# Optimization experiments

Measured on AMD Instinct MI355X. Metric: run time of the kernel, lower is better.

The kernel has to match this reference:

```python
import jax, jax.numpy as jnp
import numpy as np


def setup_inputs() -> dict:
    key = jax.random.key(0)
    k_xyz, k_w1, k_b1, k_w2, k_b2 = jax.random.split(key, 5)
    B, N = 2, 1024
    D_MODEL, N_HEADS = 128, 8
    HID = D_MODEL // 2
    # Kaiming-ish init scale for the tiny MLP weights
    return {
        "xyz": jax.random.normal(k_xyz, (B, 3, N), dtype=jnp.float32),
        "W1": jax.random.normal(k_w1, (3, HID), dtype=jnp.float32) * (1.0 / np.sqrt(3.0)),
        "b1": jax.random.normal(k_b1, (HID,), dtype=jnp.float32) * 0.01,
        "W2": jax.random.normal(k_w2, (HID, N_HEADS), dtype=jnp.float32) * (1.0 / np.sqrt(HID)),
        "b2": jax.random.normal(k_b2, (N_HEADS,), dtype=jnp.float32) * 0.01,
    }


def reference(xyz, W1, b1, W2, b2):
    # xyz: [B, 3, N] -> [B, N, 3]
    pts = jnp.transpose(xyz, (0, 2, 1))
    # pairwise relative positions: rel[b, i, j, :] = pts[b, j] - pts[b, i]
    # (matches xyz.unsqueeze(1) - xyz.unsqueeze(2) in torch)
    rel = pts[:, None, :, :] - pts[:, :, None, :]          # [B, N, N, 3]
    h = jax.nn.relu(jnp.einsum("bijc,ch->bijh", rel, W1) + b1)  # [B, N, N, HID]
    bias = jnp.einsum("bijh,hk->bijk", h, W2) + b2         # [B, N, N, H]
    # permute(0, 3, 1, 2) -> [B, H, N, N]
    return jnp.transpose(bias, (0, 3, 1, 2))
```

## Files before the change

kernel.cpp:

```cpp
#include <hip/hip_runtime.h>
#include <hip/hip_bf16.h>

#define HID   64
#define NHD   8
#define IT    16
#define WAVES 8
#define JTW   32
#define JT    (WAVES*JTW)

typedef _Float16 f16x8 __attribute__((ext_vector_type(8)));
typedef float    f32x4 __attribute__((ext_vector_type(4)));

__global__ __launch_bounds__(WAVES * 64, 4) void relposenc_f16(
    const float* __restrict__ xyz, const float* __restrict__ W1,
    const float* __restrict__ b1,  const float* __restrict__ W2,
    const float* __restrict__ b2,  float* __restrict__ out, int N) {

  __shared__ float    sW1b1[4][HID];
  __shared__ _Float16 sU[IT][HID];

  const int tid  = threadIdx.x;
  const int wave = tid >> 6;
  const int lane = tid & 63;
  const int col  = lane & 15;
  const int hgrp = lane >> 4;
  const int b    = blockIdx.z;
  const int i0   = blockIdx.y * IT;
  const int j0   = blockIdx.x * JT + wave * JTW;

  const float* xb = xyz + (size_t)b * 3 * N;

  if (tid < 4 * HID) {
    int r = tid >> 6, h = tid & 63;
    sW1b1[r][h] = (r < 3) ? W1[r * HID + h] : b1[h];
  }
  for (int t = tid; t < IT * HID; t += WAVES * 64) {
    int ii = t >> 6, h = t & 63;
    int i  = i0 + ii;
    float u = fmaf(xb[i], W1[h],
              fmaf(xb[N + i], W1[HID + h],
                   xb[2 * N + i] * W1[2 * HID + h]));
    sU[ii][h] = (_Float16)u;
  }

  f16x8 aLo[2], aHi[2];
  #pragma unroll
  for (int kb = 0; kb < 2; ++kb)
    #pragma unroll
    for (int e = 0; e < 8; ++e) {
      int h = kb * 32 + hgrp * 8 + e;
      aLo[kb][e] = (_Float16)((col < NHD)  ? W2[h * NHD + col]       : 0.f);
      aHi[kb][e] = (_Float16)((col >= NHD) ? W2[h * NHD + (col - 8)] : 0.f);
    }
  float b2v[4];
  #pragma unroll
  for (int r = 0; r < 4; ++r) b2v[r] = b2[((hgrp & 1) << 2) + r];

  __syncthreads();

  f16x8 aj[2][2];
  #pragma unroll
  for (int t = 0; t < 2; ++t) {
    int j = j0 + t * 16 + col;
    float x0 = xb[j], x1 = xb[N + j], x2 = xb[2 * N + j];
    #pragma unroll
    for (int kb = 0; kb < 2; ++kb)
      #pragma unroll
      for (int e = 0; e < 8; ++e) {
        int h = kb * 32 + hgrp * 8 + e;
        float v = fmaf(x0, sW1b1[0][h],
                  fmaf(x1, sW1b1[1][h],
                  fmaf(x2, sW1b1[2][h], sW1b1[3][h])));
        aj[t][kb][e] = (_Float16)v;
      }
  }

  const size_t jj = (size_t)j0 + col + ((size_t)(lane >> 5) << 4);
  const int kbase = (hgrp & 1) << 2;
  float* outp = out + ((size_t)(b * NHD + kbase) * N + i0) * N + jj;
  const size_t plane = (size_t)N * N;

  const f16x8 z = {0, 0, 0, 0, 0, 0, 0, 0};

  f16x8 nu0 = *(const f16x8*)&sU[0][hgrp * 8];
  f16x8 nu1 = *(const f16x8*)&sU[0][32 + hgrp * 8];

  for (int ii = 0; ii < IT; ++ii) {
    f16x8 u0 = nu0, u1 = nu1;
    if (ii + 1 < IT) {
      nu0 = *(const f16x8*)&sU[ii + 1][hgrp * 8];
      nu1 = *(const f16x8*)&sU[ii + 1][32 + hgrp * 8];
    }

    f16x8 d00 = __builtin_elementwise_max(aj[0][0] - u0, z);
    f16x8 d01 = __builtin_elementwise_max(aj[0][1] - u1, z);
    f16x8 d10 = __builtin_elementwise_max(aj[1][0] - u0, z);
    f16x8 d11 = __builtin_elementwise_max(aj[1][1] - u1, z);

    f32x4 cA = {0.f, 0.f, 0.f, 0.f}, cB = {0.f, 0.f, 0.f, 0.f};
    cA = __builtin_amdgcn_mfma_f32_16x16x32_f16(aLo[0], d00, cA, 0, 0, 0);
    cA = __builtin_amdgcn_mfma_f32_16x16x32_f16(aLo[1], d01, cA, 0, 0, 0);
    cB = __builtin_amdgcn_mfma_f32_16x16x32_f16(aHi[0], d10, cB, 0, 0, 0);
    cB = __builtin_amdgcn_mfma_f32_16x16x32_f16(aHi[1], d11, cB, 0, 0, 0);

    float* p = outp + (size_t)ii * N;
    #pragma unroll
    for (int r = 0; r < 4; ++r) {
      p[(size_t)r * plane] = cA[r] + cB[r] + b2v[r];
    }
  }
}

extern "C" void kernel_launch(void* const* d_in, const int* in_sizes, int n_in,
                              void* d_out, int out_size, void* d_ws, size_t ws_size,
                              hipStream_t stream) {
  const float* xyz = (const float*)d_in[0];
  const float* W1  = (const float*)d_in[1];
  const float* b1  = (const float*)d_in[2];
  const float* W2  = (const float*)d_in[3];
  const float* b2  = (const float*)d_in[4];
  float* out = (float*)d_out;

  const long long in0 = in_sizes[0];
  const int N = (int)((3LL * (long long)out_size) / (8LL * in0));
  const int B = (int)(in0 / (3LL * N));

  dim3 grid(N / JT, N / IT, B);
  relposenc_f16<<<grid, WAVES * 64, 0, stream>>>(xyz, W1, b1, W2, b2, out, N);
}
```

Before: 24.28 us.

## Stage output rows in LDS and write full rows with coalesced 16-byte stores

Each block now covers 2 query rows across all N columns. Results go into a 64KB LDS buffer laid out head-major, and each wave then streams one head's rows to global memory as contiguous float4 stores. Before, lanes issued scattered 4-byte stores. The j-side first layer is now computed with packed f16 FMAs (W1 and b1 held in registers), and b2 is folded into the accumulator init. The large LDS footprint caps occupancy, the j-projection is recomputed for every pair of rows, and the NFIX=1024 LDS size hardcodes N.

New measurement: 35.71 us. 47.0% more time.

```diff
diff --git a/kernel.cpp b/kernel.cpp
--- a/kernel.cpp
+++ b/kernel.cpp
@@ -3,20 +3,19 @@
 
 #define HID   64
 #define NHD   8
-#define IT    16
+#define IT    2
 #define WAVES 8
-#define JTW   32
-#define JT    (WAVES*JTW)
+#define NFIX  1024
 
 typedef _Float16 f16x8 __attribute__((ext_vector_type(8)));
 typedef float    f32x4 __attribute__((ext_vector_type(4)));
 
-__global__ __launch_bounds__(WAVES * 64, 4) void relposenc_f16(
+__global__ __launch_bounds__(WAVES * 64, 4) void relposenc_lds(
     const float* __restrict__ xyz, const float* __restrict__ W1,
     const float* __restrict__ b1,  const float* __restrict__ W2,
     const float* __restrict__ b2,  float* __restrict__ out, int N) {
 
-  __shared__ float    sW1b1[4][HID];
+  __shared__ float    sOut[NHD][IT][NFIX];
   __shared__ _Float16 sU[IT][HID];
 
   const int tid  = threadIdx.x;
@@ -24,24 +23,31 @@
   const int lane = tid & 63;
   const int col  = lane & 15;
   const int hgrp = lane >> 4;
-  const int b    = blockIdx.z;
-  const int i0   = blockIdx.y * IT;
-  const int j0   = blockIdx.x * JT + wave * JTW;
+  const int b    = blockIdx.y;
+  const int i0   = blockIdx.x * IT;
 
   const float* xb = xyz + (size_t)b * 3 * N;
 
-  if (tid < 4 * HID) {
-    int r = tid >> 6, h = tid & 63;
-    sW1b1[r][h] = (r < 3) ? W1[r * HID + h] : b1[h];
-  }
-  for (int t = tid; t < IT * HID; t += WAVES * 64) {
-    int ii = t >> 6, h = t & 63;
+  if (tid < IT * HID) {
+    int ii = tid >> 6, h = tid & 63;
     int i  = i0 + ii;
     float u = fmaf(xb[i], W1[h],
               fmaf(xb[N + i], W1[HID + h],
                    xb[2 * N + i] * W1[2 * HID + h]));
     sU[ii][h] = (_Float16)u;
   }
+
+  f16x8 w1f[2][3], bbf[2];
+  #pragma unroll
+  for (int kb = 0; kb < 2; ++kb)
+    #pragma unroll
+    for (int e = 0; e < 8; ++e) {
+      int h = kb * 32 + hgrp * 8 + e;
+      w1f[kb][0][e] = (_Float16)W1[h];
+      w1f[kb][1][e] = (_Float16)W1[HID + h];
+      w1f[kb][2][e] = (_Float16)W1[2 * HID + h];
+      bbf[kb][e]    = (_Float16)b1[h];
+    }
 
   f16x8 aLo[2], aHi[2];
   #pragma unroll
@@ -52,61 +58,73 @@
       aLo[kb][e] = (_Float16)((col < NHD)  ? W2[h * NHD + col]       : 0.f);
       aHi[kb][e] = (_Float16)((col >= NHD) ? W2[h * NHD + (col - 8)] : 0.f);
     }
+  const int kbase = (hgrp & 1) << 2;
   float b2v[4];
   #pragma unroll
-  for (int r = 0; r < 4; ++r) b2v[r] = b2[((hgrp & 1) << 2) + r];
+  for (int r = 0; r < 4; ++r) b2v[r] = b2[kbase + r];
 
   __syncthreads();
 
-  f16x8 aj[2][2];
+  f16x8 uf[IT][2];
   #pragma unroll
-  for (int t = 0; t < 2; ++t) {
-    int j = j0 + t * 16 + col;
-    float x0 = xb[j], x1 = xb[N + j], x2 = xb[2 * N + j];
+  for (int ii = 0; ii < IT; ++ii)
     #pragma unroll
     for (int kb = 0; kb < 2; ++kb)
+      uf[ii][kb] = *(const f16x8*)&sU[ii][kb * 32 + hgrp * 8];
+
+  const int jloc   = col + ((lane >> 5) << 4);
+  const int ngroup = N / (WAVES * 32);
+  const f16x8 z = {0, 0, 0, 0, 0, 0, 0, 0};
+
+  for (int g = 0; g < ngroup; ++g) {
+    const int jbase = (wave * ngroup + g) * 32;
+
+    f16x8 aj[2][2];
+    #pragma unroll
+    for (int t = 0; t < 2; ++t) {
+      int j = jbase + t * 16 + col;
+      f16x8 x0 = (_Float16)xb[j];
+      f16x8 x1 = (_Float16)xb[N + j];
+      f16x8 x2 = (_Float16)xb[2 * N + j];
       #pragma unroll
-      for (int e = 0; e < 8; ++e) {
-        int h = kb * 32 + hgrp * 8 + e;
-        float v = fmaf(x0, sW1b1[0][h],
-                  fmaf(x1, sW1b1[1][h],
-                  fmaf(x2, sW1b1[2][h], sW1b1[3][h])));
-        aj[t][kb][e] = (_Float16)v;
-      }
+      for (int kb = 0; kb < 2; ++kb)
+        aj[t][kb] = __builtin_elementwise_fma(x0, w1f[kb][0],
+                    __builtin_elementwise_fma(x1, w1f[kb][1],
+                    __builtin_elementwise_fma(x2, w1f[kb][2], bbf[kb])));
+    }
+
+    #pragma unroll
+    for (int ii = 0; ii < IT; ++ii) {
+      f16x8 d00 = __builtin_elementwise_max(aj[0][0] - uf[ii][0], z);
+      f16x8 d01 = __builtin_elementwise_max(aj[0][1] - uf[ii][1], z);
+      f16x8 d10 = __builtin_elementwise_max(aj[1][0] - uf[ii][0], z);
+      f16x8 d11 = __builtin_elementwise_max(aj[1][1] - uf[ii][1], z);
+
+      f32x4 cA = {b2v[0], b2v[1], b2v[2], b2v[3]};
+      f32x4 cB = {0.f, 0.f, 0.f, 0.f};
+      cA = __builtin_amdgcn_mfma_f32_16x16x32_f16(aLo[0], d00, cA, 0, 0, 0);
+      cA = __builtin_amdgcn_mfma_f32_16x16x32_f16(aLo[1], d01, cA, 0, 0, 0);
+      cB = __builtin_amdgcn_mfma_f32_16x16x32_f16(aHi[0], d10, cB, 0, 0, 0);
+      cB = __builtin_amdgcn_mfma_f32_16x16x32_f16(aHi[1], d11, cB, 0, 0, 0);
+
+      const int jj = jbase + jloc;
+      #pragma unroll
+      for (int r = 0; r < 4; ++r)
+        sOut[kbase + r][ii][jj] = cA[r] + cB[r];
+    }
   }
 
-  const size_t jj = (size_t)j0 + col + ((size_t)(lane >> 5) << 4);
-  const int kbase = (hgrp & 1) << 2;
-  float* outp = out + ((size_t)(b * NHD + kbase) * N + i0) * N + jj;
-  const size_t plane = (size_t)N * N;
+  __syncthreads();
 
-  const f16x8 z = {0, 0, 0, 0, 0, 0, 0, 0};
-
-  f16x8 nu0 = *(const f16x8*)&sU[0][hgrp * 8];
-  f16x8 nu1 = *(const f16x8*)&sU[0][32 + hgrp * 8];
-
-  for (int ii = 0; ii < IT; ++ii) {
-    f16x8 u0 = nu0, u1 = nu1;
-    if (ii + 1 < IT) {
-      nu0 = *(const f16x8*)&sU[ii + 1][hgrp * 8];
-      nu1 = *(const f16x8*)&sU[ii + 1][32 + hgrp * 8];
-    }
-
-    f16x8 d00 = __builtin_elementwise_max(aj[0][0] - u0, z);
-    f16x8 d01 = __builtin_elementwise_max(aj[0][1] - u1, z);
-    f16x8 d10 = __builtin_elementwise_max(aj[1][0] - u0, z);
-    f16x8 d11 = __builtin_elementwise_max(aj[1][1] - u1, z);
-
-    f32x4 cA = {0.f, 0.f, 0.f, 0.f}, cB = {0.f, 0.f, 0.f, 0.f};
-    cA = __builtin_amdgcn_mfma_f32_16x16x32_f16(aLo[0], d00, cA, 0, 0, 0);
-    cA = __builtin_amdgcn_mfma_f32_16x16x32_f16(aLo[1], d01, cA, 0, 0, 0);
-    cB = __builtin_amdgcn_mfma_f32_16x16x32_f16(aHi[0], d10, cB, 0, 0, 0);
-    cB = __builtin_amdgcn_mfma_f32_16x16x32_f16(aHi[1], d11, cB, 0, 0, 0);
-
-    float* p = outp + (size_t)ii * N;
+  {
+    const float* src = &sOut[wave][0][0];
+    float* dst = out + (((size_t)(b * NHD + wave)) * N + i0) * N;
+    const int total = IT * N;
     #pragma unroll
-    for (int r = 0; r < 4; ++r) {
-      p[(size_t)r * plane] = cA[r] + cB[r] + b2v[r];
+    for (int it = 0; it < total / 256; ++it) {
+      int off = it * 256 + lane * 4;
+      f32x4 v = *(const f32x4*)(src + off);
+      *(f32x4*)(dst + off) = v;
     }
   }
 }
@@ -125,6 +143,6 @@
   const int N = (int)((3LL * (long long)out_size) / (8LL * in0));
   const int B = (int)(in0 / (3LL * N));
 
-  dim3 grid(N / JT, N / IT, B);
-  relposenc_f16<<<grid, WAVES * 64, 0, stream>>>(xyz, W1, b1, W2, b2, out, N);
+  dim3 grid(N / IT, B);
+  relposenc_lds<<<grid, WAVES * 64, 0, stream>>>(xyz, W1, b1, W2, b2, out, N);
 }
```

## Swap MFMA operand roles so each lane stores contiguous float4 outputs

Applied to the files above, without the earlier changes.

The MFMA now takes the ReLU activations as the A operand and W2 as the B operand, so each lane's four accumulator rows map to four consecutive j positions of a single head. This lets each lane write 16-byte vector stores instead of four scalar stores spread over separate head planes, and the b2 bias is folded into the accumulator's initial value. W2 and b2 are staged through shared memory and the software prefetch of the sU rows is removed. Half the lanes (col >= 8) compute padding columns and their stores are masked off, so MFMA output utilisation is unchanged while store efficiency should improve.

After: 21.23 us. 12.6% less time.

```diff
diff --git a/kernel.cpp b/kernel.cpp
--- a/kernel.cpp
+++ b/kernel.cpp
@@ -1,5 +1,4 @@
 #include <hip/hip_runtime.h>
-#include <hip/hip_bf16.h>
 
 #define HID   64
 #define NHD   8
@@ -11,12 +10,14 @@
 typedef _Float16 f16x8 __attribute__((ext_vector_type(8)));
 typedef float    f32x4 __attribute__((ext_vector_type(4)));
 
-__global__ __launch_bounds__(WAVES * 64, 4) void relposenc_f16(
+__global__ __launch_bounds__(WAVES * 64, 4) void relposenc_x4(
     const float* __restrict__ xyz, const float* __restrict__ W1,
     const float* __restrict__ b1,  const float* __restrict__ W2,
     const float* __restrict__ b2,  float* __restrict__ out, int N) {
 
   __shared__ float    sW1b1[4][HID];
+  __shared__ float    sW2p[HID][NHD + 1];
+  __shared__ float    sB2[NHD];
   __shared__ _Float16 sU[IT][HID];
 
   const int tid  = threadIdx.x;
@@ -30,10 +31,12 @@
 
   const float* xb = xyz + (size_t)b * 3 * N;
 
+  sW2p[tid >> 3][tid & 7] = W2[tid];
   if (tid < 4 * HID) {
     int r = tid >> 6, h = tid & 63;
     sW1b1[r][h] = (r < 3) ? W1[r * HID + h] : b1[h];
   }
+  if (tid < NHD) sB2[tid] = b2[tid];
   for (int t = tid; t < IT * HID; t += WAVES * 64) {
     int ii = t >> 6, h = t & 63;
     int i  = i0 + ii;
@@ -43,20 +46,17 @@
     sU[ii][h] = (_Float16)u;
   }
 
-  f16x8 aLo[2], aHi[2];
+  __syncthreads();
+
+  f16x8 w2f[2];
   #pragma unroll
   for (int kb = 0; kb < 2; ++kb)
     #pragma unroll
     for (int e = 0; e < 8; ++e) {
       int h = kb * 32 + hgrp * 8 + e;
-      aLo[kb][e] = (_Float16)((col < NHD)  ? W2[h * NHD + col]       : 0.f);
-      aHi[kb][e] = (_Float16)((col >= NHD) ? W2[h * NHD + (col - 8)] : 0.f);
+      w2f[kb][e] = (_Float16)((col < NHD) ? sW2p[h][col] : 0.f);
     }
-  float b2v[4];
-  #pragma unroll
-  for (int r = 0; r < 4; ++r) b2v[r] = b2[((hgrp & 1) << 2) + r];
-
-  __syncthreads();
+  const float b2s = sB2[col & 7];
 
   f16x8 aj[2][2];
   #pragma unroll
@@ -75,38 +75,31 @@
       }
   }
 
-  const size_t jj = (size_t)j0 + col + ((size_t)(lane >> 5) << 4);
-  const int kbase = (hgrp & 1) << 2;
-  float* outp = out + ((size_t)(b * NHD + kbase) * N + i0) * N + jj;
-  const size_t plane = (size_t)N * N;
+  const size_t baseOff =
+      ((size_t)(b * NHD + (col & 7)) * N + i0) * N + j0 + hgrp * 4;
 
   const f16x8 z = {0, 0, 0, 0, 0, 0, 0, 0};
 
-  f16x8 nu0 = *(const f16x8*)&sU[0][hgrp * 8];
-  f16x8 nu1 = *(const f16x8*)&sU[0][32 + hgrp * 8];
-
   for (int ii = 0; ii < IT; ++ii) {
-    f16x8 u0 = nu0, u1 = nu1;
-    if (ii + 1 < IT) {
-      nu0 = *(const f16x8*)&sU[ii + 1][hgrp * 8];
-      nu1 = *(const f16x8*)&sU[ii + 1][32 + hgrp * 8];
-    }
+    f16x8 u0 = *(const f16x8*)&sU[ii][hgrp * 8];
+    f16x8 u1 = *(const f16x8*)&sU[ii][32 + hgrp * 8];
 
     f16x8 d00 = __builtin_elementwise_max(aj[0][0] - u0, z);
     f16x8 d01 = __builtin_elementwise_max(aj[0][1] - u1, z);
     f16x8 d10 = __builtin_elementwise_max(aj[1][0] - u0, z);
     f16x8 d11 = __builtin_elementwise_max(aj[1][1] - u1, z);
 
-    f32x4 cA = {0.f, 0.f, 0.f, 0.f}, cB = {0.f, 0.f, 0.f, 0.f};
-    cA = __builtin_amdgcn_mfma_f32_16x16x32_f16(aLo[0], d00, cA, 0, 0, 0);
-    cA = __builtin_amdgcn_mfma_f32_16x16x32_f16(aLo[1], d01, cA, 0, 0, 0);
-    cB = __builtin_amdgcn_mfma_f32_16x16x32_f16(aHi[0], d10, cB, 0, 0, 0);
-    cB = __builtin_amdgcn_mfma_f32_16x16x32_f16(aHi[1], d11, cB, 0, 0, 0);
+    f32x4 c0 = {b2s, b2s, b2s, b2s};
+    f32x4 c1 = {b2s, b2s, b2s, b2s};
+    c0 = __builtin_amdgcn_mfma_f32_16x16x32_f16(d00, w2f[0], c0, 0, 0, 0);
+    c0 = __builtin_amdgcn_mfma_f32_16x16x32_f16(d01, w2f[1], c0, 0, 0, 0);
+    c1 = __builtin_amdgcn_mfma_f32_16x16x32_f16(d10, w2f[0], c1, 0, 0, 0);
+    c1 = __builtin_amdgcn_mfma_f32_16x16x32_f16(d11, w2f[1], c1, 0, 0, 0);
 
-    float* p = outp + (size_t)ii * N;
-    #pragma unroll
-    for (int r = 0; r < 4; ++r) {
-      p[(size_t)r * plane] = cA[r] + cB[r] + b2v[r];
+    if (col < NHD) {
+      float* p = out + baseOff + (size_t)ii * N;
+      *(f32x4*)p        = c0;
+      *(f32x4*)(p + 16) = c1;
     }
   }
 }
@@ -126,5 +119,5 @@
   const int B = (int)(in0 / (3LL * N));
 
   dim3 grid(N / JT, N / IT, B);
-  relposenc_f16<<<grid, WAVES * 64, 0, stream>>>(xyz, W1, b1, W2, b2, out, N);
+  relposenc_x4<<<grid, WAVES * 64, 0, stream>>>(xyz, W1, b1, W2, b2, out, N);
 }
```
